# Performance work log

Hardware: AMD Instinct MI355X
Metric: run time of the kernel (lower is better)

Reference implementation:

```python
import jax, jax.numpy as jnp
import numpy as np

NEG_SLOPE = 0.2  # PyG GATConv default leaky_relu slope


def _gat_layer(x, src, dst, W, a_src, a_dst, b, N, concat):
    # x: [N, F_in]; W: [F_in, H*C]; a_src/a_dst: [H, C]; b: [H*C] or [C]
    H, C = a_src.shape
    h = (x @ W).reshape(N, H, C)                      # [N, H, C]
    al_s = jnp.einsum('nhc,hc->nh', h, a_src)          # [N, H]
    al_d = jnp.einsum('nhc,hc->nh', h, a_dst)          # [N, H]
    e = jax.nn.leaky_relu(al_s[src] + al_d[dst], NEG_SLOPE)  # [E, H]
    # segment softmax over incoming edges of each dst node
    m = jax.ops.segment_max(e, dst, num_segments=N)    # [N, H]
    ex = jnp.exp(e - m[dst])                           # [E, H]
    denom = jax.ops.segment_sum(ex, dst, num_segments=N)
    attn = ex / denom[dst]                             # [E, H]
    msg = (h[src] * attn[:, :, None]).reshape(-1, H * C)  # [E, H*C]
    out = jax.ops.segment_sum(msg, dst, num_segments=N)   # [N, H*C]
    if concat:
        return out + b
    return out.reshape(N, H, C).mean(axis=1) + b


def setup_inputs() -> dict:
    key = jax.random.key(0)
    ks = jax.random.split(key, 20)
    N, E, D, C, H = 20000, 160000, 768, 128, 4
    HC = H * C  # 512
    def glorot(k, shape):
        fan = shape[0] + shape[-1]
        return jax.random.uniform(k, shape, jnp.float32, -1.0, 1.0) * np.sqrt(6.0 / fan)
    inp = {
        'x': jax.random.normal(ks[0], (N, D), jnp.float32),
        'edge_index': jax.random.randint(ks[1], (2, E), 0, N, jnp.int64),
        'W1': glorot(ks[2], (D, HC)),  'as1': glorot(ks[3], (H, C)), 'ad1': glorot(ks[4], (H, C)), 'b1': jnp.zeros((HC,), jnp.float32),
        'W2': glorot(ks[5], (HC, HC)), 'as2': glorot(ks[6], (H, C)), 'ad2': glorot(ks[7], (H, C)), 'b2': jnp.zeros((HC,), jnp.float32),
        'W3': glorot(ks[8], (HC, C)),  'as3': glorot(ks[9], (1, C)), 'ad3': glorot(ks[10], (1, C)), 'b3': jnp.zeros((C,), jnp.float32),
        'Ws1': glorot(ks[11], (C, C // 2)), 'bs1': jnp.zeros((C // 2,), jnp.float32),
        'Ws2': glorot(ks[12], (C // 2, 1)), 'bs2': jnp.zeros((1,), jnp.float32),
    }
    return inp


def reference(x, edge_index, W1, as1, ad1, b1, W2, as2, ad2, b2, W3, as3, ad3, b3, Ws1, bs1, Ws2, bs2):
    N = x.shape[0]
    loops = jnp.arange(N, dtype=edge_index.dtype)
    src = jnp.concatenate([edge_index[0], loops])  # add self-loops (PyG default)
    dst = jnp.concatenate([edge_index[1], loops])
    h = _gat_layer(x, src, dst, W1, as1, ad1, b1, N, concat=True)
    h = jax.nn.relu(h)  # dropout is identity in eval mode
    h = _gat_layer(h, src, dst, W2, as2, ad2, b2, N, concat=True)
    h = jax.nn.relu(h)
    h = _gat_layer(h, src, dst, W3, as3, ad3, b3, N, concat=False)
    # risk scoring head: Linear -> ReLU -> Linear -> Sigmoid
    s = jax.nn.relu(h @ Ws1 + bs1)
    return jax.nn.sigmoid(s @ Ws2 + bs2)  # [N, 1]
```

## Files before the change

### kernel.cpp

```cpp
#include <hip/hip_runtime.h>
#include <hip/hip_bf16.h>
#include <math.h>

#define NEG_SLOPE 0.2f

typedef __attribute__((ext_vector_type(8))) __bf16 bf16x8;
typedef __attribute__((ext_vector_type(4))) float f32x4;

__device__ inline float lrelu(float v) { return v > 0.f ? v : NEG_SLOPE * v; }

__device__ inline unsigned short f2bf(float f) {
    __hip_bfloat16 h = __float2bfloat16(f);
    return *reinterpret_cast<unsigned short*>(&h);
}
__device__ inline float bf_lo(unsigned u) { return __uint_as_float(u << 16); }
__device__ inline float bf_hi(unsigned u) { return __uint_as_float(u & 0xffff0000u); }

__device__ inline void chunk_stats(float v, float& m, float& den, float& wl, float& so) {
    float mc = v;
#pragma unroll
    for (int d = 1; d < 64; d <<= 1) mc = fmaxf(mc, __shfl_xor(mc, d));
    float pl = __expf(v - mc);
    float dc = pl;
#pragma unroll
    for (int d = 1; d < 64; d <<= 1) dc += __shfl_xor(dc, d);
    float nm = fmaxf(m, mc);
    so = __expf(m - nm);
    float sc = __expf(mc - nm);
    den = den * so + dc * sc;
    m = nm;
    wl = pl * sc;
}

__global__ void count_deg_kernel(const int* __restrict__ ei, int E, int N,
                                 int* __restrict__ deg) {
    int e = blockIdx.x * blockDim.x + threadIdx.x;
    if (e >= E + N) return;
    int dst = (e < E) ? ei[E + e] : (e - E);
    atomicAdd(&deg[dst], 1);
}

__global__ void scan_kernel(const int* __restrict__ deg, int* __restrict__ off, int N) {
    __shared__ int sums[1024];
    int tid = threadIdx.x;
    int chunk = (N + 1023) / 1024;
    int start = tid * chunk;
    int end = start + chunk; if (end > N) end = N;
    int s = 0;
    for (int i = start; i < end && i < N; i++) s += deg[i];
    sums[tid] = s;
    __syncthreads();
    for (int d = 1; d < 1024; d <<= 1) {
        int v = 0;
        if (tid >= d) v = sums[tid - d];
        __syncthreads();
        if (tid >= d) sums[tid] += v;
        __syncthreads();
    }
    int prefix = (tid == 0) ? 0 : sums[tid - 1];
    int run = prefix;
    for (int i = start; i < end && i < N; i++) { off[i] = run; run += deg[i]; }
    if (tid == 1023) off[N] = sums[1023];
}

__global__ void scatter_kernel(const int* __restrict__ ei, int E, int N,
                               const int* __restrict__ off, int* __restrict__ cursor,
                               int* __restrict__ csr_src) {
    int e = blockIdx.x * blockDim.x + threadIdx.x;
    if (e >= E + N) return;
    int src, dst;
    if (e < E) { src = ei[e]; dst = ei[E + e]; }
    else       { src = dst = e - E; }
    int pos = off[dst] + atomicAdd(&cursor[dst], 1);
    csr_src[pos] = src;
}

__global__ void cast_bf16_kernel(const float* __restrict__ in, unsigned short* __restrict__ out,
                                 size_t n4) {
    size_t i = (size_t)blockIdx.x * blockDim.x + threadIdx.x;
    if (i >= n4) return;
    float4 v = reinterpret_cast<const float4*>(in)[i];
    ushort4 o;
    o.x = f2bf(v.x); o.y = f2bf(v.y); o.z = f2bf(v.z); o.w = f2bf(v.w);
    reinterpret_cast<ushort4*>(out)[i] = o;
}

__global__ void transpose_cast_kernel(const float* __restrict__ in, unsigned short* __restrict__ out,
                                      int K, int N) {
    int idx = blockIdx.x * blockDim.x + threadIdx.x;
    if (idx >= K * N) return;
    int n = idx / K, k = idx % K;
    out[(size_t)n * K + k] = f2bf(in[(size_t)k * N + n]);
}

template <int HEADS>
__global__ __launch_bounds__(256) void gemm_bf16_alpha(const unsigned short* __restrict__ A,
                                                       const unsigned short* __restrict__ Bt,
                                                       unsigned short* __restrict__ C,
                                                       int M, int N, int K, int rowTiles,
                                                       const float* __restrict__ a_src,
                                                       const float* __restrict__ a_dst,
                                                       float* __restrict__ alS,
                                                       float* __restrict__ alD) {
    __shared__ unsigned short Asl[64 * 64];
    __shared__ unsigned short Bsl[128 * 64];
    const int tid  = threadIdx.x;
    const int lane = tid & 63;
    const int wave = tid >> 6;

    int r, c;
    {
        int b = blockIdx.x;
        int colTiles = N >> 7;
        if (colTiles == 4) {
            int mainRows = rowTiles & ~7;
            int mainBlocks = mainRows * 4;
            if (b < mainBlocks) {
                int xcd = b & 7;
                c = (b >> 3) & 3;
                r = (b >> 5) * 8 + xcd;
            } else {
                int idx = b - mainBlocks;
                r = mainRows + (idx >> 2);
                c = idx & 3;
            }
        } else { r = b; c = 0; }
    }
    const int rowBase = r * 64;
    const int colBase = c * 128;
    const int wm = (wave & 1) * 32;
    const int wn = (wave >> 1) * 64;
    const int q   = lane >> 4;
    const int l16 = lane & 15;

    const int r0 = tid >> 3;
    const int cg = (tid & 7) ^ (r0 & 7);

    f32x4 acc[2][4] = {};

    for (int k0 = 0; k0 < K; k0 += 64) {
#pragma unroll
        for (int it = 0; it < 2; it++) {
            int s = it * 256 + tid;
            int rr = it * 32 + r0;
            int ga = rowBase + rr; if (ga >= M) ga = M - 1;
            const unsigned short* gpa = A + (size_t)ga * K + k0 + cg * 8;
            __builtin_amdgcn_global_load_lds(
                (const __attribute__((address_space(1))) void*)gpa,
                (__attribute__((address_space(3))) void*)&Asl[(size_t)s * 8],
                16, 0, 0);
        }
#pragma unroll
        for (int it = 0; it < 4; it++) {
            int s = it * 256 + tid;
            int rr = it * 32 + r0;
            const unsigned short* gpb = Bt + (size_t)(colBase + rr) * K + k0 + cg * 8;
            __builtin_amdgcn_global_load_lds(
                (const __attribute__((address_space(1))) void*)gpb,
                (__attribute__((address_space(3))) void*)&Bsl[(size_t)s * 8],
                16, 0, 0);
        }
        __syncthreads();

#pragma unroll
        for (int kh = 0; kh < 2; kh++) {
            bf16x8 af[2], bfv[4];
#pragma unroll
            for (int mi = 0; mi < 2; mi++) {
                int row = wm + mi * 16 + l16;
                int ch = (kh * 4 + q) ^ (row & 7);
                af[mi] = *reinterpret_cast<const bf16x8*>(&Asl[row * 64 + ch * 8]);
            }
#pragma unroll
            for (int ni = 0; ni < 4; ni++) {
                int row = wn + ni * 16 + l16;
                int ch = (kh * 4 + q) ^ (row & 7);
                bfv[ni] = *reinterpret_cast<const bf16x8*>(&Bsl[row * 64 + ch * 8]);
            }
#pragma unroll
            for (int mi = 0; mi < 2; mi++)
#pragma unroll
                for (int ni = 0; ni < 4; ni++)
                    acc[mi][ni] = __builtin_amdgcn_mfma_f32_16x16x32_bf16(af[mi], bfv[ni], acc[mi][ni], 0, 0, 0);
        }
        __syncthreads();
    }

    const int hIdx = colBase >> 7;
    const float* asl = a_src + hIdx * 128;
    const float* adl = a_dst + hIdx * 128;
    float acoef[4], dcoef[4];
#pragma unroll
    for (int ni = 0; ni < 4; ni++) {
        int cl = wn + ni * 16 + l16;
        acoef[ni] = asl[cl];
        dcoef[ni] = adl[cl];
    }

    float2* red = reinterpret_cast<float2*>(Asl);
    const int half = wn >> 6;

#pragma unroll
    for (int mi = 0; mi < 2; mi++) {
#pragma unroll
        for (int rr = 0; rr < 4; rr++) {
            int lrow = wm + mi * 16 + q * 4 + rr;
            int grow = rowBase + lrow;
            bool ok = grow < M;
            float vs = 0.f, vd = 0.f;
#pragma unroll
            for (int ni = 0; ni < 4; ni++) {
                float hv = acc[mi][ni][rr];
                vs += hv * acoef[ni];
                vd += hv * dcoef[ni];
                if (ok) {
                    int gcol = colBase + wn + ni * 16 + l16;
                    C[(size_t)grow * N + gcol] = f2bf(hv);
                }
            }
#pragma unroll
            for (int d = 1; d < 16; d <<= 1) {
                vs += __shfl_xor(vs, d);
                vd += __shfl_xor(vd, d);
            }
            if (l16 == 0) red[lrow * 2 + half] = make_float2(vs, vd);
        }
    }
    __syncthreads();
    if (tid < 64) {
        int grow = rowBase + tid;
        if (grow < M) {
            float2 a = red[tid * 2 + 0];
            float2 b = red[tid * 2 + 1];
            alS[(size_t)grow * HEADS + hIdx] = a.x + b.x;
            alD[(size_t)grow * HEADS + hIdx] = a.y + b.y;
        }
    }
}

template <int H, int C, int MODE>
__global__ __launch_bounds__(256) void gat_aggregate(const unsigned short* __restrict__ hb,
                                                     const float* __restrict__ alS,
                                                     const float* __restrict__ alD,
                                                     const int* __restrict__ off,
                                                     const int* __restrict__ csr_src,
                                                     const float* __restrict__ bias,
                                                     void* __restrict__ outbuf,
                                                     const float* __restrict__ Ws1,
                                                     const float* __restrict__ bs1,
                                                     const float* __restrict__ Ws2,
                                                     const float* __restrict__ bs2,
                                                     int N) {
    constexpr int HC = H * C;
    constexpr int PER = HC / 64;
    __shared__ int   sIdx[4][64];
    __shared__ float sW[4][H][68];

    int n = (blockIdx.x * blockDim.x + threadIdx.x) >> 6;
    int lane = threadIdx.x & 63;
    int wave = threadIdx.x >> 6;
    if (n >= N) return;
    int beg = off[n], end = off[n + 1];

    float ad0 = 0.f, ad1 = 0.f, ad2 = 0.f, ad3 = 0.f;
    if (H == 4) {
        float4 t = *reinterpret_cast<const float4*>(&alD[n * 4]);
        ad0 = t.x; ad1 = t.y; ad2 = t.z; ad3 = t.w;
    } else {
        ad0 = alD[n];
    }

    const int myh = (lane * PER) / C;
    const unsigned short* hbl = hb + (size_t)lane * PER;
    const float* sWrow = &sW[wave][0][0] + (size_t)myh * 68;

    float m0 = -1e30f, m1 = -1e30f, m2 = -1e30f, m3 = -1e30f;
    float dn0 = 0.f, dn1 = 0.f, dn2 = 0.f, dn3 = 0.f;
    float acc0 = 0.f, acc1 = 0.f, acc2 = 0.f, acc3 = 0.f,
          acc4 = 0.f, acc5 = 0.f, acc6 = 0.f, acc7 = 0.f;

    for (int base = beg; base < end; base += 64) {
        int cnt = end - base; if (cnt > 64) cnt = 64;
        bool act = lane < cnt;
        int s_l = csr_src[act ? (base + lane) : base];

        float v0 = -1e30f, v1 = -1e30f, v2 = -1e30f, v3 = -1e30f;
        if (H == 4) {
            float4 a4 = *reinterpret_cast<const float4*>(&alS[s_l * 4]);
            v0 = act ? lrelu(a4.x + ad0) : -1e30f;
            v1 = act ? lrelu(a4.y + ad1) : -1e30f;
            v2 = act ? lrelu(a4.z + ad2) : -1e30f;
            v3 = act ? lrelu(a4.w + ad3) : -1e30f;
        } else {
            v0 = act ? lrelu(alS[s_l] + ad0) : -1e30f;
        }

        float wl0 = 0.f, wl1 = 0.f, wl2 = 0.f, wl3 = 0.f;
        float so0 = 0.f, so1 = 0.f, so2 = 0.f, so3 = 0.f;
        chunk_stats(v0, m0, dn0, wl0, so0);
        if (H == 4) {
            chunk_stats(v1, m1, dn1, wl1, so1);
            chunk_stats(v2, m2, dn2, wl2, so2);
            chunk_stats(v3, m3, dn3, wl3, so3);
        }
        sIdx[wave][lane] = s_l;
        sW[wave][0][lane] = wl0;
        if (H == 4) {
            sW[wave][1][lane] = wl1;
            sW[wave][2][lane] = wl2;
            sW[wave][3][lane] = wl3;
        }

        float sAcc;
        if (H == 4) {
            float rlo = (myh & 1) ? so1 : so0;
            float rhi = (myh & 1) ? so3 : so2;
            sAcc = (myh & 2) ? rhi : rlo;
        } else sAcc = so0;
        acc0 *= sAcc; acc1 *= sAcc;
        if (PER == 8) {
            acc2 *= sAcc; acc3 *= sAcc; acc4 *= sAcc; acc5 *= sAcc;
            acc6 *= sAcc; acc7 *= sAcc;
        }

        int cntR = (cnt + 3) & ~3;

        if (PER == 8) {
            int4   sI = *reinterpret_cast<const int4*>(&sIdx[wave][0]);
            float4 wv = *reinterpret_cast<const float4*>(&sWrow[0]);
            uint4 gA0 = *reinterpret_cast<const uint4*>(hbl + (size_t)sI.x * HC);
            uint4 gA1 = *reinterpret_cast<const uint4*>(hbl + (size_t)sI.y * HC);
            uint4 gA2 = *reinterpret_cast<const uint4*>(hbl + (size_t)sI.z * HC);
            uint4 gA3 = *reinterpret_cast<const uint4*>(hbl + (size_t)sI.w * HC);
            for (int i = 0; i < cntR; i += 4) {
                int4 sI2 = {}; float4 wv2 = {};
                uint4 gB0 = {}, gB1 = {}, gB2 = {}, gB3 = {};
                if (i + 4 < cntR) {
                    sI2 = *reinterpret_cast<const int4*>(&sIdx[wave][i + 4]);
                    wv2 = *reinterpret_cast<const float4*>(&sWrow[i + 4]);
                    gB0 = *reinterpret_cast<const uint4*>(hbl + (size_t)sI2.x * HC);
                    gB1 = *reinterpret_cast<const uint4*>(hbl + (size_t)sI2.y * HC);
                    gB2 = *reinterpret_cast<const uint4*>(hbl + (size_t)sI2.z * HC);
                    gB3 = *reinterpret_cast<const uint4*>(hbl + (size_t)sI2.w * HC);
                }
#define CONSUME(G, W)                                                   \
                { uint4 rc = G; float w = W;                            \
                  acc0 += bf_lo(rc.x) * w; acc1 += bf_hi(rc.x) * w;     \
                  acc2 += bf_lo(rc.y) * w; acc3 += bf_hi(rc.y) * w;     \
                  acc4 += bf_lo(rc.z) * w; acc5 += bf_hi(rc.z) * w;     \
                  acc6 += bf_lo(rc.w) * w; acc7 += bf_hi(rc.w) * w; }
                CONSUME(gA0, wv.x); CONSUME(gA1, wv.y);
                CONSUME(gA2, wv.z); CONSUME(gA3, wv.w);
#undef CONSUME
                sI = sI2; wv = wv2;
                gA0 = gB0; gA1 = gB1; gA2 = gB2; gA3 = gB3;
            }
        } else {
            int4   sI = *reinterpret_cast<const int4*>(&sIdx[wave][0]);
            float4 wv = *reinterpret_cast<const float4*>(&sWrow[0]);
            unsigned gA0 = *reinterpret_cast<const unsigned*>(hbl + (size_t)sI.x * HC);
            unsigned gA1 = *reinterpret_cast<const unsigned*>(hbl + (size_t)sI.y * HC);
            unsigned gA2 = *reinterpret_cast<const unsigned*>(hbl + (size_t)sI.z * HC);
            unsigned gA3 = *reinterpret_cast<const unsigned*>(hbl + (size_t)sI.w * HC);
            for (int i = 0; i < cntR; i += 4) {
                int4 sI2 = {}; float4 wv2 = {};
                unsigned gB0 = 0, gB1 = 0, gB2 = 0, gB3 = 0;
                if (i + 4 < cntR) {
                    sI2 = *reinterpret_cast<const int4*>(&sIdx[wave][i + 4]);
                    wv2 = *reinterpret_cast<const float4*>(&sWrow[i + 4]);
                    gB0 = *reinterpret_cast<const unsigned*>(hbl + (size_t)sI2.x * HC);
                    gB1 = *reinterpret_cast<const unsigned*>(hbl + (size_t)sI2.y * HC);
                    gB2 = *reinterpret_cast<const unsigned*>(hbl + (size_t)sI2.z * HC);
                    gB3 = *reinterpret_cast<const unsigned*>(hbl + (size_t)sI2.w * HC);
                }
                acc0 += bf_lo(gA0) * wv.x; acc1 += bf_hi(gA0) * wv.x;
                acc0 += bf_lo(gA1) * wv.y; acc1 += bf_hi(gA1) * wv.y;
                acc0 += bf_lo(gA2) * wv.z; acc1 += bf_hi(gA2) * wv.z;
                acc0 += bf_lo(gA3) * wv.w; acc1 += bf_hi(gA3) * wv.w;
                sI = sI2; wv = wv2;
                gA0 = gB0; gA1 = gB1; gA2 = gB2; gA3 = gB3;
            }
        }
    }

    float invd;
    if (H == 4) {
        float rlo = (myh & 1) ? dn1 : dn0;
        float rhi = (myh & 1) ? dn3 : dn2;
        invd = 1.f / ((myh & 2) ? rhi : rlo);
    } else invd = 1.f / dn0;

    if (MODE == 0) {
        unsigned short* op = (unsigned short*)outbuf + (size_t)n * HC + lane * PER;
        const float* bp = bias + lane * PER;
        if (PER == 8) {
            op[0] = f2bf(fmaxf(acc0 * invd + bp[0], 0.f));
            op[1] = f2bf(fmaxf(acc1 * invd + bp[1], 0.f));
            op[2] = f2bf(fmaxf(acc2 * invd + bp[2], 0.f));
            op[3] = f2bf(fmaxf(acc3 * invd + bp[3], 0.f));
            op[4] = f2bf(fmaxf(acc4 * invd + bp[4], 0.f));
            op[5] = f2bf(fmaxf(acc5 * invd + bp[5], 0.f));
            op[6] = f2bf(fmaxf(acc6 * invd + bp[6], 0.f));
            op[7] = f2bf(fmaxf(acc7 * invd + bp[7], 0.f));
        } else {
            op[0] = f2bf(fmaxf(acc0 * invd + bp[0], 0.f));
            op[1] = f2bf(fmaxf(acc1 * invd + bp[1], 0.f));
        }
    } else {
        float h0 = acc0 * invd + bias[2 * lane];
        float h1 = acc1 * invd + bias[2 * lane + 1];
        float s = 0.f;
#pragma unroll
        for (int k = 0; k < 64; k++) {
            float a = __shfl(h0, k);
            float b = __shfl(h1, k);
            s += a * Ws1[(2 * k) * 64 + lane];
            s += b * Ws1[(2 * k + 1) * 64 + lane];
        }
        s = fmaxf(s + bs1[lane], 0.f);
        float z = s * Ws2[lane];
#pragma unroll
        for (int d = 1; d < 64; d <<= 1) z += __shfl_xor(z, d);
        if (lane == 0) ((float*)outbuf)[n] = 1.f / (1.f + __expf(-(z + bs2[0])));
    }
}

extern "C" void kernel_launch(void* const* d_in, const int* in_sizes, int n_in,
                              void* d_out, int out_size, void* d_ws, size_t ws_size,
                              hipStream_t stream) {
    const float* x   = (const float*)d_in[0];
    const int*   ei  = (const int*)d_in[1];
    const float* W1  = (const float*)d_in[2];
    const float* as1 = (const float*)d_in[3];
    const float* ad1 = (const float*)d_in[4];
    const float* b1  = (const float*)d_in[5];
    const float* W2  = (const float*)d_in[6];
    const float* as2 = (const float*)d_in[7];
    const float* ad2 = (const float*)d_in[8];
    const float* b2  = (const float*)d_in[9];
    const float* W3  = (const float*)d_in[10];
    const float* as3 = (const float*)d_in[11];
    const float* ad3 = (const float*)d_in[12];
    const float* b3  = (const float*)d_in[13];
    const float* Ws1 = (const float*)d_in[14];
    const float* bs1 = (const float*)d_in[15];
    const float* Ws2 = (const float*)d_in[16];
    const float* bs2 = (const float*)d_in[17];

    const int N = out_size;
    const int E = in_sizes[1] / 2;
    const int D = in_sizes[0] / N;
    const int HC = 512, H = 4, C = 128;
    const int Etot = E + N;

    char* p = (char*)d_ws;
    auto alloc = [&](size_t bytes) -> void* {
        void* q = (void*)p;
        p += (bytes + 255) & ~(size_t)255;
        return q;
    };
    char*  zbeg   = p;
    int*   deg    = (int*)alloc((size_t)N * 4);
    int*   cursor = (int*)alloc((size_t)N * 4);
    char*  zend   = p;
    float* alS1   = (float*)alloc((size_t)N * H * 4);
    float* alD1   = (float*)alloc((size_t)N * H * 4);
    float* alS2   = (float*)alloc((size_t)N * H * 4);
    float* alD2   = (float*)alloc((size_t)N * H * 4);
    float* alS3   = (float*)alloc((size_t)N * 4);
    float* alD3   = (float*)alloc((size_t)N * 4);
    int*   off    = (int*)alloc((size_t)(N + 1) * 4);
    int*   csr    = (int*)alloc((size_t)Etot * 4);
    unsigned short* hbuf = (unsigned short*)alloc((size_t)N * HC * 2);
    unsigned short* xbf  = (unsigned short*)alloc((size_t)N * D * 2);
    unsigned short* obf  = (unsigned short*)alloc((size_t)N * HC * 2);
    unsigned short* W1t  = (unsigned short*)alloc((size_t)D * HC * 2);
    unsigned short* W2t  = (unsigned short*)alloc((size_t)HC * HC * 2);
    unsigned short* W3t  = (unsigned short*)alloc((size_t)HC * C * 2);

    hipMemsetAsync(zbeg, 0, (size_t)(zend - zbeg), stream);

    const int tb = 256;
    count_deg_kernel<<<(Etot + tb - 1) / tb, tb, 0, stream>>>(ei, E, N, deg);
    scan_kernel<<<1, 1024, 0, stream>>>(deg, off, N);
    scatter_kernel<<<(Etot + tb - 1) / tb, tb, 0, stream>>>(ei, E, N, off, cursor, csr);

    {
        size_t n4 = (size_t)N * D / 4;
        cast_bf16_kernel<<<(int)((n4 + 255) / 256), 256, 0, stream>>>(x, xbf, n4);
        transpose_cast_kernel<<<(D * HC + 255) / 256, 256, 0, stream>>>(W1, W1t, D, HC);
        transpose_cast_kernel<<<(HC * HC + 255) / 256, 256, 0, stream>>>(W2, W2t, HC, HC);
        transpose_cast_kernel<<<(HC * C + 255) / 256, 256, 0, stream>>>(W3, W3t, HC, C);
    }

    int node_blocks = (N + 3) / 4;
    int rowTiles64 = (N + 63) / 64;

    gemm_bf16_alpha<4><<<rowTiles64 * 4, 256, 0, stream>>>(
        xbf, W1t, hbuf, N, HC, D, rowTiles64, as1, ad1, alS1, alD1);
    gat_aggregate<4, 128, 0><<<node_blocks, 256, 0, stream>>>(
        hbuf, alS1, alD1, off, csr, b1, obf, nullptr, nullptr, nullptr, nullptr, N);

    gemm_bf16_alpha<4><<<rowTiles64 * 4, 256, 0, stream>>>(
        obf, W2t, hbuf, N, HC, HC, rowTiles64, as2, ad2, alS2, alD2);
    gat_aggregate<4, 128, 0><<<node_blocks, 256, 0, stream>>>(
        hbuf, alS2, alD2, off, csr, b2, obf, nullptr, nullptr, nullptr, nullptr, N);

    gemm_bf16_alpha<1><<<rowTiles64, 256, 0, stream>>>(
        obf, W3t, hbuf, N, C, HC, rowTiles64, as3, ad3, alS3, alD3);
    gat_aggregate<1, 128, 1><<<node_blocks, 256, 0, stream>>>(
        hbuf, alS3, alD3, off, csr, b3, (float*)d_out, Ws1, bs1, Ws2, bs2, N);
}
```

Baseline: 358.0 us.

## Split aggregation softmax into per-head 16-lane groups and move scoring head to MFMA

The aggregation kernel now handles 16 edges per chunk. Each 16-lane group owns one head and computes a single online softmax with 4-step shuffle reductions, replacing four 64-lane reductions per chunk. With an average in-degree of about 9, most nodes should need only one chunk and far fewer shuffles and exps. The third layer now writes bf16 output, and a new tiled MFMA kernel computes the Linear-ReLU-Linear-Sigmoid head, replacing the per-node shuffle-heavy scalar loop. The cost is an extra launch and extra bf16 rounding of the third-layer output before the head.

```diff
diff --git a/kernel.cpp b/kernel.cpp
--- a/kernel.cpp
+++ b/kernel.cpp
@@ -15,22 +15,6 @@
 }
 __device__ inline float bf_lo(unsigned u) { return __uint_as_float(u << 16); }
 __device__ inline float bf_hi(unsigned u) { return __uint_as_float(u & 0xffff0000u); }
-
-__device__ inline void chunk_stats(float v, float& m, float& den, float& wl, float& so) {
-    float mc = v;
-#pragma unroll
-    for (int d = 1; d < 64; d <<= 1) mc = fmaxf(mc, __shfl_xor(mc, d));
-    float pl = __expf(v - mc);
-    float dc = pl;
-#pragma unroll
-    for (int d = 1; d < 64; d <<= 1) dc += __shfl_xor(dc, d);
-    float nm = fmaxf(m, mc);
-    so = __expf(m - nm);
-    float sc = __expf(mc - nm);
-    den = den * so + dc * sc;
-    m = nm;
-    wl = pl * sc;
-}
 
 __global__ void count_deg_kernel(const int* __restrict__ ei, int E, int N,
                                  int* __restrict__ deg) {
@@ -245,16 +229,12 @@
                                                      const int* __restrict__ off,
                                                      const int* __restrict__ csr_src,
                                                      const float* __restrict__ bias,
-                                                     void* __restrict__ outbuf,
-                                                     const float* __restrict__ Ws1,
-                                                     const float* __restrict__ bs1,
-                                                     const float* __restrict__ Ws2,
-                                                     const float* __restrict__ bs2,
+                                                     unsigned short* __restrict__ outbuf,
                                                      int N) {
     constexpr int HC = H * C;
     constexpr int PER = HC / 64;
-    __shared__ int   sIdx[4][64];
-    __shared__ float sW[4][H][68];
+    __shared__ int   sIdx[4][16];
+    __shared__ float sW[4][64];
 
     int n = (blockIdx.x * blockDim.x + threadIdx.x) >> 6;
     int lane = threadIdx.x & 63;
@@ -262,65 +242,44 @@
     if (n >= N) return;
     int beg = off[n], end = off[n + 1];
 
-    float ad0 = 0.f, ad1 = 0.f, ad2 = 0.f, ad3 = 0.f;
-    if (H == 4) {
-        float4 t = *reinterpret_cast<const float4*>(&alD[n * 4]);
-        ad0 = t.x; ad1 = t.y; ad2 = t.z; ad3 = t.w;
-    } else {
-        ad0 = alD[n];
-    }
-
-    const int myh = (lane * PER) / C;
+    const int grp  = lane >> 4;
+    const int slot = lane & 15;
+    const int myh  = (H == 4) ? grp : 0;
+    const float adh = alD[n * H + myh];
     const unsigned short* hbl = hb + (size_t)lane * PER;
-    const float* sWrow = &sW[wave][0][0] + (size_t)myh * 68;
-
-    float m0 = -1e30f, m1 = -1e30f, m2 = -1e30f, m3 = -1e30f;
-    float dn0 = 0.f, dn1 = 0.f, dn2 = 0.f, dn3 = 0.f;
+    const float* sWrow = &sW[wave][grp * 16];
+
+    float m = -1e30f, dn = 0.f;
     float acc0 = 0.f, acc1 = 0.f, acc2 = 0.f, acc3 = 0.f,
           acc4 = 0.f, acc5 = 0.f, acc6 = 0.f, acc7 = 0.f;
 
-    for (int base = beg; base < end; base += 64) {
-        int cnt = end - base; if (cnt > 64) cnt = 64;
-        bool act = lane < cnt;
-        int s_l = csr_src[act ? (base + lane) : base];
-
-        float v0 = -1e30f, v1 = -1e30f, v2 = -1e30f, v3 = -1e30f;
-        if (H == 4) {
-            float4 a4 = *reinterpret_cast<const float4*>(&alS[s_l * 4]);
-            v0 = act ? lrelu(a4.x + ad0) : -1e30f;
-            v1 = act ? lrelu(a4.y + ad1) : -1e30f;
-            v2 = act ? lrelu(a4.z + ad2) : -1e30f;
-            v3 = act ? lrelu(a4.w + ad3) : -1e30f;
-        } else {
-            v0 = act ? lrelu(alS[s_l] + ad0) : -1e30f;
-        }
-
-        float wl0 = 0.f, wl1 = 0.f, wl2 = 0.f, wl3 = 0.f;
-        float so0 = 0.f, so1 = 0.f, so2 = 0.f, so3 = 0.f;
-        chunk_stats(v0, m0, dn0, wl0, so0);
-        if (H == 4) {
-            chunk_stats(v1, m1, dn1, wl1, so1);
-            chunk_stats(v2, m2, dn2, wl2, so2);
-            chunk_stats(v3, m3, dn3, wl3, so3);
-        }
-        sIdx[wave][lane] = s_l;
-        sW[wave][0][lane] = wl0;
-        if (H == 4) {
-            sW[wave][1][lane] = wl1;
-            sW[wave][2][lane] = wl2;
-            sW[wave][3][lane] = wl3;
-        }
-
-        float sAcc;
-        if (H == 4) {
-            float rlo = (myh & 1) ? so1 : so0;
-            float rhi = (myh & 1) ? so3 : so2;
-            sAcc = (myh & 2) ? rhi : rlo;
-        } else sAcc = so0;
-        acc0 *= sAcc; acc1 *= sAcc;
+    for (int base = beg; base < end; base += 16) {
+        int cnt = end - base; if (cnt > 16) cnt = 16;
+        bool act = slot < cnt;
+        int s_l = csr_src[act ? (base + slot) : base];
+        float v = act ? lrelu(alS[s_l * H + myh] + adh) : -1e30f;
+
+        float mc = v;
+#pragma unroll
+        for (int d = 1; d < 16; d <<= 1) mc = fmaxf(mc, __shfl_xor(mc, d));
+        float pl = __expf(v - mc);
+        float dc = pl;
+#pragma unroll
+        for (int d = 1; d < 16; d <<= 1) dc += __shfl_xor(dc, d);
+        float nm = fmaxf(m, mc);
+        float so = __expf(m - nm);
+        float sc = __expf(mc - nm);
+        dn = dn * so + dc * sc;
+        m = nm;
+        float wl = pl * sc;
+
+        if (lane < 16) sIdx[wave][lane] = s_l;
+        sW[wave][lane] = wl;
+
+        acc0 *= so; acc1 *= so;
         if (PER == 8) {
-            acc2 *= sAcc; acc3 *= sAcc; acc4 *= sAcc; acc5 *= sAcc;
-            acc6 *= sAcc; acc7 *= sAcc;
+            acc2 *= so; acc3 *= so; acc4 *= so; acc5 *= so;
+            acc6 *= so; acc7 *= so;
         }
 
         int cntR = (cnt + 3) & ~3;
@@ -383,45 +342,113 @@
         }
     }
 
-    float invd;
-    if (H == 4) {
-        float rlo = (myh & 1) ? dn1 : dn0;
-        float rhi = (myh & 1) ? dn3 : dn2;
-        invd = 1.f / ((myh & 2) ? rhi : rlo);
-    } else invd = 1.f / dn0;
-
-    if (MODE == 0) {
-        unsigned short* op = (unsigned short*)outbuf + (size_t)n * HC + lane * PER;
-        const float* bp = bias + lane * PER;
-        if (PER == 8) {
-            op[0] = f2bf(fmaxf(acc0 * invd + bp[0], 0.f));
-            op[1] = f2bf(fmaxf(acc1 * invd + bp[1], 0.f));
-            op[2] = f2bf(fmaxf(acc2 * invd + bp[2], 0.f));
-            op[3] = f2bf(fmaxf(acc3 * invd + bp[3], 0.f));
-            op[4] = f2bf(fmaxf(acc4 * invd + bp[4], 0.f));
-            op[5] = f2bf(fmaxf(acc5 * invd + bp[5], 0.f));
-            op[6] = f2bf(fmaxf(acc6 * invd + bp[6], 0.f));
-            op[7] = f2bf(fmaxf(acc7 * invd + bp[7], 0.f));
-        } else {
-            op[0] = f2bf(fmaxf(acc0 * invd + bp[0], 0.f));
-            op[1] = f2bf(fmaxf(acc1 * invd + bp[1], 0.f));
-        }
+    float invd = 1.f / dn;
+    unsigned short* op = outbuf + (size_t)n * HC + lane * PER;
+    const float* bp = bias + lane * PER;
+    if (PER == 8) {
+        float o0 = acc0 * invd + bp[0], o1 = acc1 * invd + bp[1];
+        float o2 = acc2 * invd + bp[2], o3 = acc3 * invd + bp[3];
+        float o4 = acc4 * invd + bp[4], o5 = acc5 * invd + bp[5];
+        float o6 = acc6 * invd + bp[6], o7 = acc7 * invd + bp[7];
+        if (MODE == 0) {
+            o0 = fmaxf(o0, 0.f); o1 = fmaxf(o1, 0.f); o2 = fmaxf(o2, 0.f); o3 = fmaxf(o3, 0.f);
+            o4 = fmaxf(o4, 0.f); o5 = fmaxf(o5, 0.f); o6 = fmaxf(o6, 0.f); o7 = fmaxf(o7, 0.f);
+        }
+        op[0] = f2bf(o0); op[1] = f2bf(o1); op[2] = f2bf(o2); op[3] = f2bf(o3);
+        op[4] = f2bf(o4); op[5] = f2bf(o5); op[6] = f2bf(o6); op[7] = f2bf(o7);
     } else {
-        float h0 = acc0 * invd + bias[2 * lane];
-        float h1 = acc1 * invd + bias[2 * lane + 1];
-        float s = 0.f;
-#pragma unroll
-        for (int k = 0; k < 64; k++) {
-            float a = __shfl(h0, k);
-            float b = __shfl(h1, k);
-            s += a * Ws1[(2 * k) * 64 + lane];
-            s += b * Ws1[(2 * k + 1) * 64 + lane];
-        }
-        s = fmaxf(s + bs1[lane], 0.f);
-        float z = s * Ws2[lane];
-#pragma unroll
-        for (int d = 1; d < 64; d <<= 1) z += __shfl_xor(z, d);
-        if (lane == 0) ((float*)outbuf)[n] = 1.f / (1.f + __expf(-(z + bs2[0])));
+        float o0 = acc0 * invd + bp[0], o1 = acc1 * invd + bp[1];
+        if (MODE == 0) { o0 = fmaxf(o0, 0.f); o1 = fmaxf(o1, 0.f); }
+        op[0] = f2bf(o0); op[1] = f2bf(o1);
+    }
+}
+
+__global__ __launch_bounds__(256) void head_mfma(const unsigned short* __restrict__ H3,
+                                                 const unsigned short* __restrict__ W1t,
+                                                 const float* __restrict__ bs1,
+                                                 const float* __restrict__ Ws2,
+                                                 const float* __restrict__ bs2,
+                                                 float* __restrict__ out, int M) {
+    __shared__ unsigned short Asl[128 * 128];
+    __shared__ unsigned short Bsl[64 * 128];
+    const int tid = threadIdx.x, lane = tid & 63, wave = tid >> 6;
+    const int q = lane >> 4, l16 = lane & 15;
+    const int rowBase = blockIdx.x * 128;
+    const int r0 = tid >> 4;
+    const int cg = (tid & 15) ^ (r0 & 7);
+
+#pragma unroll
+    for (int it = 0; it < 8; it++) {
+        int s = it * 256 + tid;
+        int r = it * 16 + r0;
+        int ga = rowBase + r; if (ga >= M) ga = M - 1;
+        const unsigned short* gp = H3 + (size_t)ga * 128 + cg * 8;
+        __builtin_amdgcn_global_load_lds(
+            (const __attribute__((address_space(1))) void*)gp,
+            (__attribute__((address_space(3))) void*)&Asl[(size_t)s * 8], 16, 0, 0);
+    }
+#pragma unroll
+    for (int it = 0; it < 4; it++) {
+        int s = it * 256 + tid;
+        int r = it * 16 + r0;
+        const unsigned short* gp = W1t + (size_t)r * 128 + cg * 8;
+        __builtin_amdgcn_global_load_lds(
+            (const __attribute__((address_space(1))) void*)gp,
+            (__attribute__((address_space(3))) void*)&Bsl[(size_t)s * 8], 16, 0, 0);
+    }
+    __syncthreads();
+
+    const int wm = wave * 32;
+    f32x4 acc[2][4] = {};
+#pragma unroll
+    for (int kh = 0; kh < 4; kh++) {
+        bf16x8 af[2], bfv[4];
+#pragma unroll
+        for (int mi = 0; mi < 2; mi++) {
+            int row = wm + mi * 16 + l16;
+            int ch = (kh * 4 + q) ^ (row & 7);
+            af[mi] = *reinterpret_cast<const bf16x8*>(&Asl[row * 128 + ch * 8]);
+        }
+#pragma unroll
+        for (int ni = 0; ni < 4; ni++) {
+            int row = ni * 16 + l16;
+            int ch = (kh * 4 + q) ^ (row & 7);
+            bfv[ni] = *reinterpret_cast<const bf16x8*>(&Bsl[row * 128 + ch * 8]);
+        }
+#pragma unroll
+        for (int mi = 0; mi < 2; mi++)
+#pragma unroll
+            for (int ni = 0; ni < 4; ni++)
+                acc[mi][ni] = __builtin_amdgcn_mfma_f32_16x16x32_bf16(af[mi], bfv[ni], acc[mi][ni], 0, 0, 0);
+    }
+    __syncthreads();
+
+    float b1v[4], w2v[4];
+#pragma unroll
+    for (int ni = 0; ni < 4; ni++) {
+        int cI = ni * 16 + l16;
+        b1v[ni] = bs1[cI];
+        w2v[ni] = Ws2[cI];
+    }
+    float* red = reinterpret_cast<float*>(Bsl);
+#pragma unroll
+    for (int mi = 0; mi < 2; mi++) {
+#pragma unroll
+        for (int r = 0; r < 4; r++) {
+            int lrow = wm + mi * 16 + q * 4 + r;
+            float p = 0.f;
+#pragma unroll
+            for (int ni = 0; ni < 4; ni++)
+                p += fmaxf(acc[mi][ni][r] + b1v[ni], 0.f) * w2v[ni];
+#pragma unroll
+            for (int d = 1; d < 16; d <<= 1) p += __shfl_xor(p, d);
+            if (l16 == 0) red[lrow] = p;
+        }
+    }
+    __syncthreads();
+    if (tid < 128) {
+        int g = rowBase + tid;
+        if (g < M) out[g] = 1.f / (1.f + __expf(-(red[tid] + bs2[0])));
     }
 }
 
@@ -477,6 +504,7 @@
     unsigned short* W1t  = (unsigned short*)alloc((size_t)D * HC * 2);
     unsigned short* W2t  = (unsigned short*)alloc((size_t)HC * HC * 2);
     unsigned short* W3t  = (unsigned short*)alloc((size_t)HC * C * 2);
+    unsigned short* Ws1t = (unsigned short*)alloc((size_t)C * 64 * 2);
 
     hipMemsetAsync(zbeg, 0, (size_t)(zend - zbeg), stream);
 
@@ -491,23 +519,27 @@
         transpose_cast_kernel<<<(D * HC + 255) / 256, 256, 0, stream>>>(W1, W1t, D, HC);
         transpose_cast_kernel<<<(HC * HC + 255) / 256, 256, 0, stream>>>(W2, W2t, HC, HC);
         transpose_cast_kernel<<<(HC * C + 255) / 256, 256, 0, stream>>>(W3, W3t, HC, C);
+        transpose_cast_kernel<<<(128 * 64 + 255) / 256, 256, 0, stream>>>(Ws1, Ws1t, 128, 64);
     }
 
     int node_blocks = (N + 3) / 4;
     int rowTiles64 = (N + 63) / 64;
+    int headTiles = (N + 127) / 128;
 
     gemm_bf16_alpha<4><<<rowTiles64 * 4, 256, 0, stream>>>(
         xbf, W1t, hbuf, N, HC, D, rowTiles64, as1, ad1, alS1, alD1);
     gat_aggregate<4, 128, 0><<<node_blocks, 256, 0, stream>>>(
-        hbuf, alS1, alD1, off, csr, b1, obf, nullptr, nullptr, nullptr, nullptr, N);
+        hbuf, alS1, alD1, off, csr, b1, obf, N);
 
     gemm_bf16_alpha<4><<<rowTiles64 * 4, 256, 0, stream>>>(
         obf, W2t, hbuf, N, HC, HC, rowTiles64, as2, ad2, alS2, alD2);
     gat_aggregate<4, 128, 0><<<node_blocks, 256, 0, stream>>>(
-        hbuf, alS2, alD2, off, csr, b2, obf, nullptr, nullptr, nullptr, nullptr, N);
+        hbuf, alS2, alD2, off, csr, b2, obf, N);
 
     gemm_bf16_alpha<1><<<rowTiles64, 256, 0, stream>>>(
         obf, W3t, hbuf, N, C, HC, rowTiles64, as3, ad3, alS3, alD3);
-    gat_aggregate<1, 128, 1><<<node_blocks, 256, 0, stream>>>(
-        hbuf, alS3, alD3, off, csr, b3, (float*)d_out, Ws1, bs1, Ws2, bs2, N);
-}
+    gat_aggregate<1, 128, 2><<<node_blocks, 256, 0, stream>>>(
+        hbuf, alS3, alD3, off, csr, b3, xbf, N);
+
+    head_mfma<<<headTiles, 256, 0, stream>>>(xbf, Ws1t, bs1, Ws2, bs2, (float*)d_out, N);
+}
```

Result: faster. 326.1 us (-8.9%).
